# Optimization experiments

Hardware: AMD Instinct MI355X
Metric: run time of the kernel (lower is better)

Reference implementation:

```python
import jax, jax.numpy as jnp
import numpy as np

B_, L_, H_ = 2, 4096, 1024
INTER, NSTATE, NGROUPS, HEADS, P, K, CHUNK = 2048, 128, 1, 32, 64, 4, 256
CONV_DIM = INTER + 2 * NGROUPS * NSTATE  # 2304
PROJ = INTER + CONV_DIM + HEADS          # 4384
LN_EPS = 1e-5


def setup_inputs() -> dict:
    key = jax.random.key(0)
    ks = jax.random.split(key, 8)
    hidden_states = jax.random.normal(ks[0], (B_, L_, H_), jnp.float32)
    in_proj_w = jax.random.normal(ks[1], (PROJ, H_), jnp.float32) * 0.02
    conv_w = jax.random.normal(ks[2], (CONV_DIM, 1, K), jnp.float32) * 0.2
    conv_b = jnp.zeros((CONV_DIM,), jnp.float32)
    # dt_bias init as in module: inv-softplus of dt ~ LogUniform(time_step_min, time_step_max)
    dt = jnp.exp(jax.random.uniform(ks[3], (HEADS,), jnp.float32)
                 * (np.log(0.1) - np.log(0.001)) + np.log(0.001))
    dt = jnp.clip(dt, 1e-4, None)
    dt_bias = dt + jnp.log(-jnp.expm1(-dt))
    A_log = jnp.log(jax.random.uniform(ks[4], (HEADS,), jnp.float32, 1.0, 16.0))
    D = jnp.ones((HEADS,), jnp.float32)
    ln_w = jnp.ones((INTER,), jnp.float32)
    ln_b = jnp.zeros((INTER,), jnp.float32)
    out_proj_w = jax.random.normal(ks[5], (H_, INTER), jnp.float32) * 0.02
    return dict(hidden_states=hidden_states, in_proj_w=in_proj_w, conv_w=conv_w,
                conv_b=conv_b, dt_bias=dt_bias, A_log=A_log, D=D,
                ln_w=ln_w, ln_b=ln_b, out_proj_w=out_proj_w)


def _segsum(x):
    # x [..., c] -> [..., c, c] lower-triangular cumulative segment sums
    T = x.shape[-1]
    cs = jnp.cumsum(x, -1)
    d = cs[..., :, None] - cs[..., None, :]
    mask = jnp.tril(jnp.ones((T, T), bool))
    return jnp.where(mask, d, -jnp.inf)


def _ssd(x, dt, A, Bm, Cm, D):
    # x [b,l,h,p], dt [b,l,h], A [h], Bm/Cm [b,l,h,n] -> y [b,l,h,p]
    b, l, h, p = x.shape
    nc = l // CHUNK
    X = (x * dt[..., None]).reshape(b, nc, CHUNK, h, p)
    Bc = Bm.reshape(b, nc, CHUNK, h, -1)
    Cc = Cm.reshape(b, nc, CHUNK, h, -1)
    dA = (dt * A).reshape(b, nc, CHUNK, h).transpose(0, 3, 1, 2)  # [b,h,nc,c]
    Acs = jnp.cumsum(dA, -1)
    Lm = jnp.exp(_segsum(dA))                                      # [b,h,nc,c,c]
    CB = jnp.einsum("bclhn,bcshn->bhcls", Cc, Bc)
    Yd = jnp.einsum("bhcls,bcshp->bclhp", CB * Lm, X)              # intra-chunk
    decay_states = jnp.exp(Acs[..., -1:] - Acs)                    # [b,h,nc,c]
    states = jnp.einsum("bclhn,bhcl,bclhp->bchpn", Bc, decay_states, X)
    chunk_decay = jnp.exp(Acs[..., -1])                            # [b,h,nc]
    n = Bc.shape[-1]

    def step(carry, inp):
        st, dec = inp
        return carry * dec[..., None, None] + st, carry

    _, prev = jax.lax.scan(step, jnp.zeros((b, h, p, n), x.dtype),
                           (jnp.moveaxis(states, 1, 0), jnp.moveaxis(chunk_decay, 2, 0)))
    prev = jnp.moveaxis(prev, 0, 1)                                # [b,nc,h,p,n]
    Yo = jnp.einsum("bclhn,bchpn,bhcl->bclhp", Cc, prev, jnp.exp(Acs))
    return (Yd + Yo).reshape(b, l, h, p) + D[None, None, :, None] * x


def reference(hidden_states, in_proj_w, conv_w, conv_b, dt_bias, A_log, D,
              ln_w, ln_b, out_proj_w):
    b, l, _ = hidden_states.shape
    proj = hidden_states @ in_proj_w.T                             # [b,l,PROJ]
    gate = proj[..., :INTER]
    xBC = proj[..., INTER:INTER + CONV_DIM]
    dt = jax.nn.softplus(proj[..., INTER + CONV_DIM:] + dt_bias)   # [b,l,heads]
    # depthwise causal conv1d + silu
    xc = jax.lax.conv_general_dilated(xBC.transpose(0, 2, 1), conv_w, (1,),
                                      [(K - 1, 0)], feature_group_count=CONV_DIM,
                                      dimension_numbers=("NCH", "OIH", "NCH"))
    xBC = jax.nn.silu(xc + conv_b[None, :, None]).transpose(0, 2, 1)
    gn = NGROUPS * NSTATE
    x = xBC[..., :INTER].reshape(b, l, HEADS, P)
    Bm = xBC[..., INTER:INTER + gn].reshape(b, l, NGROUPS, NSTATE)
    Cm = xBC[..., INTER + gn:].reshape(b, l, NGROUPS, NSTATE)
    rep = HEADS // NGROUPS
    Bm = jnp.repeat(Bm, rep, axis=2)
    Cm = jnp.repeat(Cm, rep, axis=2)
    A = -jnp.exp(A_log)
    y = _ssd(x, dt, A, Bm, Cm, D).reshape(b, l, INTER)
    mu = y.mean(-1, keepdims=True)
    var = ((y - mu) ** 2).mean(-1, keepdims=True)
    yn = (y - mu) * jax.lax.rsqrt(var + LN_EPS) * ln_w + ln_b
    out = (yn * jax.nn.silu(gate.astype(jnp.float32))) @ out_proj_w.T
    return out
```

## Files before the change

kernel.cpp:

```cpp
#include <hip/hip_runtime.h>

typedef unsigned short u16;
typedef u16 u16x4 __attribute__((ext_vector_type(4)));
typedef u16 u16x8 __attribute__((ext_vector_type(8)));
typedef __bf16 bf16x8 __attribute__((ext_vector_type(8)));
typedef float f32x4 __attribute__((ext_vector_type(4)));

#define B_    2
#define L_    4096
#define H_    1024
#define INTER 2048
#define NSTATE 128
#define HEADS 32
#define P_    64
#define CHUNK 256
#define NC    16
#define CONVD 2304
#define PROJ  4384
#define PROJP 4480
#define XBCW  2432
#define MTOK  8192

__device__ __forceinline__ u16 f2bf(float f) {
  unsigned u = __float_as_uint(f);
  u += 0x7fffu + ((u >> 16) & 1u);
  return (u16)(u >> 16);
}
__device__ __forceinline__ float bf2f(u16 u) {
  return __uint_as_float(((unsigned)u) << 16);
}
__device__ __forceinline__ bf16x8 asbf(u16x8 v) {
  union { u16x8 u; bf16x8 b; } x; x.u = v; return x.b;
}

__global__ void cast_bf16_k(const float* __restrict__ in, u16* __restrict__ out) {
  size_t i = ((size_t)blockIdx.x * 256 + threadIdx.x) * 4;
  float4 v = *(const float4*)(in + i);
  u16x4 o = { f2bf(v.x), f2bf(v.y), f2bf(v.z), f2bf(v.w) };
  *(u16x4*)(out + i) = o;
}

__global__ void cast_w1_k(const float* __restrict__ in, u16* __restrict__ out) {
  size_t i = ((size_t)blockIdx.x * 256 + threadIdx.x) * 4;
  u16x4 o = { 0, 0, 0, 0 };
  if (i < (size_t)PROJ * H_) {
    float4 v = *(const float4*)(in + i);
    o = (u16x4){ f2bf(v.x), f2bf(v.y), f2bf(v.z), f2bf(v.w) };
  }
  *(u16x4*)(out + i) = o;
}

template<int SPLIT>
__global__ __launch_bounds__(256) void gemm_bt_k(
    const u16* __restrict__ A, const u16* __restrict__ Bm, float* __restrict__ C,
    u16* __restrict__ gateb, float* __restrict__ xbcf,
    const int K, const int ldc) {
  __shared__ u16 Als[4096];
  __shared__ u16 Bls[4096];
  const int tid = threadIdx.x;
  const int bn = blockIdx.x, bm = blockIdx.y;
  const u16* Ab = A + (size_t)bm * 128 * K;
  const u16* Bb = Bm + (size_t)bn * 128 * K;
  const int row = tid >> 2, col = (tid & 3) << 3;
  const int lane = tid & 63;
  const int wr = ((tid >> 7) & 1) << 6;
  const int wc = ((tid >> 6) & 1) << 6;
  const int fr = lane & 15;
  const int fk = (lane >> 4) << 3;
  f32x4 acc[4][4] = {};
  const size_t rA0 = (size_t)row * K + col, rA1 = (size_t)(row + 64) * K + col;
  u16x8 ra0 = *(const u16x8*)(Ab + rA0);
  u16x8 ra1 = *(const u16x8*)(Ab + rA1);
  u16x8 rb0 = *(const u16x8*)(Bb + rA0);
  u16x8 rb1 = *(const u16x8*)(Bb + rA1);
  const int nk = K >> 5;
  for (int kt = 0; kt < nk; ++kt) {
    *(u16x8*)(Als + tid * 8) = ra0;
    *(u16x8*)(Als + 2048 + tid * 8) = ra1;
    *(u16x8*)(Bls + tid * 8) = rb0;
    *(u16x8*)(Bls + 2048 + tid * 8) = rb1;
    __syncthreads();
    if (kt + 1 < nk) {
      const size_t ko = (size_t)(kt + 1) * 32;
      ra0 = *(const u16x8*)(Ab + rA0 + ko);
      ra1 = *(const u16x8*)(Ab + rA1 + ko);
      rb0 = *(const u16x8*)(Bb + rA0 + ko);
      rb1 = *(const u16x8*)(Bb + rA1 + ko);
    }
    bf16x8 af[4], bfv[4];
#pragma unroll
    for (int m = 0; m < 4; ++m)
      af[m] = asbf(*(const u16x8*)(Als + (wr + m * 16 + fr) * 32 + fk));
#pragma unroll
    for (int n = 0; n < 4; ++n)
      bfv[n] = asbf(*(const u16x8*)(Bls + (wc + n * 16 + fr) * 32 + fk));
#pragma unroll
    for (int m = 0; m < 4; ++m)
#pragma unroll
      for (int n = 0; n < 4; ++n)
        acc[m][n] = __builtin_amdgcn_mfma_f32_16x16x32_bf16(af[m], bfv[n], acc[m][n], 0, 0, 0);
    __syncthreads();
  }
  const int crow = bm * 128 + wr + ((lane >> 4) << 2);
  if (SPLIT == 0) {
    float* Cp = C + (size_t)crow * ldc + bn * 128 + wc + fr;
#pragma unroll
    for (int m = 0; m < 4; ++m)
#pragma unroll
      for (int n = 0; n < 4; ++n)
#pragma unroll
        for (int j = 0; j < 4; ++j)
          Cp[(size_t)(m * 16 + j) * ldc + n * 16] = acc[m][n][j];
  } else if (bn < 16) {
    u16* Gp = gateb + (size_t)crow * INTER + bn * 128 + wc + fr;
#pragma unroll
    for (int m = 0; m < 4; ++m)
#pragma unroll
      for (int n = 0; n < 4; ++n)
#pragma unroll
        for (int j = 0; j < 4; ++j)
          Gp[(size_t)(m * 16 + j) * INTER + n * 16] = f2bf(acc[m][n][j]);
  } else {
    float* Xp = xbcf + (size_t)crow * XBCW + (bn - 16) * 128 + wc + fr;
#pragma unroll
    for (int m = 0; m < 4; ++m)
#pragma unroll
      for (int n = 0; n < 4; ++n)
#pragma unroll
        for (int j = 0; j < 4; ++j)
          Xp[(size_t)(m * 16 + j) * XBCW + n * 16] = acc[m][n][j];
  }
}

__global__ __launch_bounds__(256) void dtpart_k(
    const float* __restrict__ hs, const float* __restrict__ w1,
    float* __restrict__ part) {
  __shared__ float hls[32 * 256];
  __shared__ float wq[32 * 8 * 32];
  const int ks = blockIdx.x, mt = blockIdx.y;
  const int m0 = mt * 32;
  const int t = threadIdx.x;
  const int h = t & 31, q = t >> 5;
  float w[32];
  {
    const float* wp = w1 + (size_t)(PROJ - HEADS + h) * H_ + ks * 256 + q * 32;
#pragma unroll
    for (int i = 0; i < 8; ++i) {
      const float4 v = *(const float4*)(wp + i * 4);
      w[i * 4] = v.x; w[i * 4 + 1] = v.y; w[i * 4 + 2] = v.z; w[i * 4 + 3] = v.w;
    }
  }
#pragma unroll
  for (int i = 0; i < 8; ++i) {
    const int idx = i * 1024 + t * 4;
    const int row = idx >> 8, col = idx & 255;
    *(float4*)(hls + idx) = *(const float4*)(hs + (size_t)(m0 + row) * H_ + ks * 256 + col);
  }
  __syncthreads();
  for (int tok = 0; tok < 32; ++tok) {
    const float* hp = hls + tok * 256 + q * 32;
    float s = 0.f;
#pragma unroll
    for (int i = 0; i < 8; ++i) {
      const float4 hv = *(const float4*)(hp + i * 4);
      s += w[i * 4] * hv.x + w[i * 4 + 1] * hv.y + w[i * 4 + 2] * hv.z + w[i * 4 + 3] * hv.w;
    }
    wq[tok * 256 + q * 32 + h] = s;
  }
  __syncthreads();
#pragma unroll
  for (int i = 0; i < 4; ++i) {
    const int idx = i * 256 + t;
    const int tok = idx >> 5, h2 = idx & 31;
    float s = 0.f;
#pragma unroll
    for (int qq = 0; qq < 8; ++qq) s += wq[tok * 256 + qq * 32 + h2];
    part[((size_t)ks * MTOK + m0 + tok) * HEADS + h2] = s;
  }
}

__global__ __launch_bounds__(256) void dtfin_k(
    const float* __restrict__ part, const float* __restrict__ dt_bias,
    float* __restrict__ dtb) {
  const int gid = blockIdx.x * 256 + threadIdx.x;
  const int h = gid & 31;
  float z = dt_bias[h];
#pragma unroll
  for (int ks = 0; ks < 4; ++ks) z += part[(size_t)ks * MTOK * HEADS + gid];
  const float sp = z > 0.f ? z + log1pf(__expf(-z)) : log1pf(__expf(z));
  dtb[gid] = sp;
}

__global__ __launch_bounds__(256) void conv_silu_k(
    const float* __restrict__ xbcf, const float* __restrict__ cw,
    const float* __restrict__ cbv,
    u16* __restrict__ xb16, float* __restrict__ Bbuf, float* __restrict__ Cbuf) {
  const int m = blockIdx.x;
  const int l = m & (L_ - 1);
  const int t = threadIdx.x;
  const float* pr = xbcf + (size_t)m * XBCW;
#pragma unroll
  for (int i = 0; i < 9; ++i) {
    const int ch = t + (i << 8);
    float acc = cbv[ch];
    const float* w = cw + ch * 4;
#pragma unroll
    for (int k = 0; k < 4; ++k) {
      const int d = k - 3;
      if (l + d >= 0) acc += w[k] * pr[(long)d * XBCW + ch];
    }
    const float v = acc / (1.f + __expf(-acc));
    if (ch < INTER) xb16[(size_t)m * INTER + ch] = f2bf(v);
    else if (ch < INTER + NSTATE) Bbuf[(size_t)m * NSTATE + (ch - INTER)] = v;
    else Cbuf[(size_t)m * NSTATE + (ch - INTER - NSTATE)] = v;
  }
}

__global__ void dtsum_k(const float* __restrict__ dtb, float* __restrict__ dts) {
  const int idx = blockIdx.x * 256 + threadIdx.x;
  const int h = idx & 31, c = (idx >> 5) & 15, b = idx >> 9;
  const float* p = dtb + (size_t)(b * L_ + c * CHUNK) * HEADS + h;
  float s = 0.f;
  for (int i = 0; i < CHUNK; ++i) s += p[(size_t)i * HEADS];
  dts[idx] = s;
}

__global__ __launch_bounds__(512) void cb_k(
    const float* __restrict__ Bbuf, const float* __restrict__ Cbuf,
    float* __restrict__ CBb) {
  __shared__ u16 Bls[CHUNK * NSTATE];
  const int bx = blockIdx.x;
  const int m0 = bx * CHUNK;
  const int t = threadIdx.x;
#pragma unroll
  for (int i = 0; i < 16; ++i) {
    const int idx = i * 2048 + t * 4;
    const int row = idx >> 7;
    const float4 v = *(const float4*)(Bbuf + (size_t)m0 * NSTATE + idx);
    u16x4 o = { f2bf(v.x), f2bf(v.y), f2bf(v.z), f2bf(v.w) };
    *(u16x4*)(Bls + (idx ^ ((row & 7) << 3))) = o;
  }
  __syncthreads();
  const int lane = t & 63, wv = t >> 6;
  const int fr = lane & 15, fu = lane >> 4;
  u16x8 afrag[2][4];
#pragma unroll
  for (int r = 0; r < 2; ++r) {
    const int row = (wv + r * 8) * 16 + fr;
    const float* cp = Cbuf + (size_t)(m0 + row) * NSTATE + fu * 8;
#pragma unroll
    for (int ks = 0; ks < 4; ++ks) {
      const float4 c0 = *(const float4*)(cp + ks * 32);
      const float4 c1 = *(const float4*)(cp + ks * 32 + 4);
      afrag[r][ks] = (u16x8){ f2bf(c0.x), f2bf(c0.y), f2bf(c0.z), f2bf(c0.w),
                              f2bf(c1.x), f2bf(c1.y), f2bf(c1.z), f2bf(c1.w) };
    }
  }
  for (int ct = 0; ct < 16; ++ct) {
    u16x8 bfrag[4];
#pragma unroll
    for (int ks = 0; ks < 4; ++ks)
      bfrag[ks] = *(const u16x8*)(Bls + (((ct * 16 + fr) * NSTATE + ks * 32 + fu * 8)
                                         ^ ((fr & 7) << 3)));
    f32x4 acc[2] = {};
#pragma unroll
    for (int r = 0; r < 2; ++r)
#pragma unroll
      for (int ks = 0; ks < 4; ++ks)
        acc[r] = __builtin_amdgcn_mfma_f32_16x16x32_bf16(asbf(afrag[r][ks]), asbf(bfrag[ks]), acc[r], 0, 0, 0);
#pragma unroll
    for (int r = 0; r < 2; ++r) {
      const int rowb = (wv + r * 8) * 16 + fu * 4;
#pragma unroll
      for (int reg = 0; reg < 4; ++reg)
        CBb[(size_t)(m0 + rowb + reg) * CHUNK + ct * 16 + fr] = acc[r][reg];
    }
  }
}

__global__ __launch_bounds__(512) void yd_states_k(
    const u16* __restrict__ xb16, const float* __restrict__ Bbuf,
    const float* __restrict__ dtb, const float* __restrict__ CBb,
    const float* __restrict__ A_log, u16* __restrict__ ydb16,
    float* __restrict__ states) {
  __shared__ float acs[CHUNK];
  __shared__ float dec[CHUNK];
  __shared__ u16 Xt[P_ * CHUNK];
  const int bx = blockIdx.x;
  const int h = bx & 31, c = (bx >> 5) & 15, b = bx >> 9;
  const int t = threadIdx.x;
  const int m0 = b * L_ + c * CHUNK;
  const float Ah = -__expf(A_log[h]);
  if (t < CHUNK) acs[t] = dtb[(size_t)(m0 + t) * HEADS + h];
  __syncthreads();
  {
#pragma unroll
    for (int i = 0; i < 4; ++i) {
      const int s = i * 64 + (t >> 3);
      const int p0 = (t & 7) * 8;
      const float dtv = acs[s];
      const u16x8 v = *(const u16x8*)(xb16 + (size_t)(m0 + s) * INTER + h * P_ + p0);
#pragma unroll
      for (int j = 0; j < 8; ++j)
        Xt[((p0 + j) * CHUNK + s) ^ (j << 3)] = f2bf(bf2f(v[j]) * dtv);
    }
  }
  for (int off = 1; off < CHUNK; off <<= 1) {
    float add = 0.f;
    if (t >= off && t < CHUNK) add = acs[t - off];
    __syncthreads();
    if (t >= off && t < CHUNK) acs[t] += add;
    __syncthreads();
  }
  {
    const float cum = (t < CHUNK) ? acs[t] : 0.f;
    const float tot = acs[CHUNK - 1];
    __syncthreads();
    if (t < CHUNK) {
      acs[t] = Ah * cum;
      dec[t] = __expf(Ah * (tot - cum));
    }
    __syncthreads();
  }
  const int lane = t & 63;
  const int wv = t >> 6;
  const int fr = lane & 15;
  const int fu = lane >> 4;
  {
    f32x4 acc_st[4] = {};
    const float* Bg = Bbuf + (size_t)m0 * NSTATE + wv * 16 + fr;
#pragma unroll 2
    for (int ks = 0; ks < 8; ++ks) {
      const int s0 = ks * 32 + fu * 8;
      u16x8 bw;
#pragma unroll
      for (int j = 0; j < 8; ++j)
        bw[j] = f2bf(Bg[(size_t)(s0 + j) * NSTATE] * dec[s0 + j]);
#pragma unroll
      for (int pt = 0; pt < 4; ++pt) {
        const int p = pt * 16 + fr;
        const u16x8 xa = *(const u16x8*)(Xt + ((p * CHUNK + s0) ^ ((p & 7) << 3)));
        acc_st[pt] = __builtin_amdgcn_mfma_f32_16x16x32_bf16(asbf(xa), asbf(bw), acc_st[pt], 0, 0, 0);
      }
    }
    float* sp = states + (size_t)((b * NC + c) * HEADS + h) * (P_ * NSTATE);
#pragma unroll
    for (int pt = 0; pt < 4; ++pt)
#pragma unroll
      for (int reg = 0; reg < 4; ++reg)
        sp[(size_t)(pt * 16 + fu * 4 + reg) * NSTATE + wv * 16 + fr] = acc_st[pt][reg];
  }
  {
#pragma unroll
    for (int rep = 0; rep < 2; ++rep) {
      const int lt = rep ? (15 - wv) : wv;
      const int l = lt * 16 + fr;
      const float acl = acs[l];
      const float* cbr = CBb + (size_t)(m0 + l) * CHUNK;
      f32x4 acc_yd[4] = {};
      const int ksn = (lt >> 1) + 1;
      for (int ks = 0; ks < ksn; ++ks) {
        const int s0 = ks * 32 + fu * 8;
        const float4 cb0 = *(const float4*)(cbr + s0);
        const float4 cb1 = *(const float4*)(cbr + s0 + 4);
        u16x8 w8;
#pragma unroll
        for (int j = 0; j < 8; ++j) {
          const int s = s0 + j;
          const float cb = j < 4 ? ((const float*)&cb0)[j] : ((const float*)&cb1)[j - 4];
          const float w = (s <= l) ? cb * __expf(acl - acs[s]) : 0.f;
          w8[j] = f2bf(w);
        }
#pragma unroll
        for (int pt = 0; pt < 4; ++pt) {
          const int p = pt * 16 + fr;
          const u16x8 xb = *(const u16x8*)(Xt + ((p * CHUNK + s0) ^ ((p & 7) << 3)));
          acc_yd[pt] = __builtin_amdgcn_mfma_f32_16x16x32_bf16(asbf(w8), asbf(xb), acc_yd[pt], 0, 0, 0);
        }
      }
#pragma unroll
      for (int pt = 0; pt < 4; ++pt)
#pragma unroll
        for (int reg = 0; reg < 4; ++reg)
          ydb16[(size_t)(m0 + lt * 16 + fu * 4 + reg) * INTER + h * P_ + pt * 16 + fr] =
              f2bf(acc_yd[pt][reg]);
    }
  }
}

__global__ void scan_k(const float* __restrict__ states, const float* __restrict__ dts,
                       const float* __restrict__ A_log, u16* __restrict__ prevb) {
  const int gid = blockIdx.x * 256 + threadIdx.x;
  const int b = gid >> 18;
  const int h = (gid >> 13) & 31;
  const int pn = gid & 8191;
  const float Ah = -__expf(A_log[h]);
  float carry = 0.f;
  const size_t base = (size_t)b * (NC * HEADS * P_ * NSTATE) + (size_t)h * (P_ * NSTATE) + pn;
  const float* sp = states + base;
  u16* pp = prevb + base;
  for (int c = 0; c < NC; ++c) {
    const float dcv = __expf(Ah * dts[(b * NC + c) * HEADS + h]);
    const float st = sp[(size_t)c * (HEADS * P_ * NSTATE)];
    pp[(size_t)c * (HEADS * P_ * NSTATE)] = f2bf(carry);
    carry = carry * dcv + st;
  }
}

__global__ __launch_bounds__(512) void yo_final_k(
    const u16* __restrict__ xb16, const float* __restrict__ Cbuf,
    const float* __restrict__ dtb, const u16* __restrict__ prevb,
    const float* __restrict__ A_log, const float* __restrict__ Dv,
    const u16* __restrict__ ydb16, u16* __restrict__ ybf) {
  __shared__ float acs[CHUNK];
  const int bx = blockIdx.x;
  const int h = bx & 31, c = (bx >> 5) & 15, b = bx >> 9;
  const int t = threadIdx.x;
  const int m0 = b * L_ + c * CHUNK;
  const float Ah = -__expf(A_log[h]);
  const float Dh = Dv[h];
  if (t < CHUNK) acs[t] = dtb[(size_t)(m0 + t) * HEADS + h];
  __syncthreads();
  for (int off = 1; off < CHUNK; off <<= 1) {
    float add = 0.f;
    if (t >= off && t < CHUNK) add = acs[t - off];
    __syncthreads();
    if (t >= off && t < CHUNK) acs[t] += add;
    __syncthreads();
  }
  const int lane = t & 63;
  const int wv = t >> 6;
  const int fr = lane & 15;
  const int fu = lane >> 4;
  const u16* pb = prevb + (size_t)((b * NC + c) * HEADS + h) * (P_ * NSTATE);
  u16x8 bfrag[4][4];
#pragma unroll
  for (int pt = 0; pt < 4; ++pt)
#pragma unroll
    for (int ks = 0; ks < 4; ++ks)
      bfrag[pt][ks] = *(const u16x8*)(pb + (pt * 16 + fr) * NSTATE + ks * 32 + fu * 8);
#pragma unroll
  for (int rep = 0; rep < 2; ++rep) {
    const int lt = rep * 8 + wv;
    const float* cr = Cbuf + (size_t)(m0 + lt * 16 + fr) * NSTATE + fu * 8;
    f32x4 acc[4] = {};
#pragma unroll
    for (int ks = 0; ks < 4; ++ks) {
      const float4 c0 = *(const float4*)(cr + ks * 32);
      const float4 c1 = *(const float4*)(cr + ks * 32 + 4);
      const u16x8 a8 = { f2bf(c0.x), f2bf(c0.y), f2bf(c0.z), f2bf(c0.w),
                         f2bf(c1.x), f2bf(c1.y), f2bf(c1.z), f2bf(c1.w) };
#pragma unroll
      for (int pt = 0; pt < 4; ++pt)
        acc[pt] = __builtin_amdgcn_mfma_f32_16x16x32_bf16(asbf(a8), asbf(bfrag[pt][ks]), acc[pt], 0, 0, 0);
    }
#pragma unroll
    for (int reg = 0; reg < 4; ++reg) {
      const int l = lt * 16 + fu * 4 + reg;
      const float el = __expf(Ah * acs[l]);
      const size_t base = (size_t)(m0 + l) * INTER + h * P_;
#pragma unroll
      for (int pt = 0; pt < 4; ++pt) {
        const int p = pt * 16 + fr;
        const float yd = bf2f(ydb16[base + p]);
        const float xv = bf2f(xb16[base + p]);
        ybf[base + p] = f2bf(yd + el * acc[pt][reg] + Dh * xv);
      }
    }
  }
}

__global__ __launch_bounds__(256) void ln_gate_k(
    const u16* __restrict__ ybf, const u16* __restrict__ gateb,
    const float* __restrict__ lnw, const float* __restrict__ lnb,
    u16* __restrict__ yact) {
  __shared__ float red[8];
  const int m = blockIdx.x, t = threadIdx.x;
  const u16x8 yv = *(const u16x8*)(ybf + (size_t)m * INTER + t * 8);
  float y[8];
  float s = 0.f, ss = 0.f;
#pragma unroll
  for (int j = 0; j < 8; ++j) { y[j] = bf2f(yv[j]); s += y[j]; ss += y[j] * y[j]; }
#pragma unroll
  for (int off = 32; off > 0; off >>= 1) {
    s += __shfl_xor(s, off);
    ss += __shfl_xor(ss, off);
  }
  if ((t & 63) == 0) { red[(t >> 6) * 2] = s; red[(t >> 6) * 2 + 1] = ss; }
  __syncthreads();
  s = red[0] + red[2] + red[4] + red[6];
  ss = red[1] + red[3] + red[5] + red[7];
  const float mu = s * (1.f / INTER);
  const float rs = rsqrtf(ss * (1.f / INTER) - mu * mu + 1e-5f);
  const u16x8 gv = *(const u16x8*)(gateb + (size_t)m * INTER + t * 8);
  const float4 w0 = *(const float4*)(lnw + t * 8);
  const float4 w1 = *(const float4*)(lnw + t * 8 + 4);
  const float4 b0 = *(const float4*)(lnb + t * 8);
  const float4 b1 = *(const float4*)(lnb + t * 8 + 4);
  const float wj[8] = { w0.x, w0.y, w0.z, w0.w, w1.x, w1.y, w1.z, w1.w };
  const float bj[8] = { b0.x, b0.y, b0.z, b0.w, b1.x, b1.y, b1.z, b1.w };
  u16x8 o;
#pragma unroll
  for (int j = 0; j < 8; ++j) {
    const float g = bf2f(gv[j]);
    const float yn = (y[j] - mu) * rs * wj[j] + bj[j];
    const float sg = g / (1.f + __expf(-g));
    o[j] = f2bf(yn * sg);
  }
  *(u16x8*)(yact + (size_t)m * INTER + t * 8) = o;
}

extern "C" void kernel_launch(void* const* d_in, const int* in_sizes, int n_in,
                              void* d_out, int out_size, void* d_ws, size_t ws_size,
                              hipStream_t stream) {
  (void)in_sizes; (void)n_in; (void)out_size; (void)ws_size;
  const float* hs     = (const float*)d_in[0];
  const float* w1     = (const float*)d_in[1];
  const float* cw     = (const float*)d_in[2];
  const float* cbv    = (const float*)d_in[3];
  const float* dtbias = (const float*)d_in[4];
  const float* alog   = (const float*)d_in[5];
  const float* Dv     = (const float*)d_in[6];
  const float* lnw    = (const float*)d_in[7];
  const float* lnb    = (const float*)d_in[8];
  const float* w2     = (const float*)d_in[9];
  float* out = (float*)d_out;
  char* ws = (char*)d_ws;
  size_t off = 0;
  auto alloc = [&](size_t bytes) {
    void* p = ws + off; off += (bytes + 255) & ~(size_t)255; return p;
  };
  u16*   hb     = (u16*)alloc((size_t)MTOK * H_ * 2);
  float* CBb    = (float*)hb;
  u16*   prevb  = hb;
  u16*   w1b    = (u16*)alloc((size_t)PROJP * H_ * 2);
  u16*   w2b    = (u16*)alloc((size_t)H_ * INTER * 2);
  u16*   gateb  = (u16*)alloc((size_t)MTOK * INTER * 2);
  float* xbcf   = (float*)alloc((size_t)MTOK * XBCW * 4);
  u16*   ydb16  = (u16*)xbcf;
  u16*   ybf    = (u16*)((char*)xbcf + ((size_t)MTOK * INTER * 2));
  u16*   xb16   = (u16*)alloc((size_t)MTOK * INTER * 2);
  u16*   yact   = xb16;
  float* Bbuf   = (float*)alloc((size_t)MTOK * NSTATE * 4);
  float* Cbuf   = (float*)alloc((size_t)MTOK * NSTATE * 4);
  float* dtb    = (float*)alloc((size_t)MTOK * HEADS * 4);
  float* dts    = (float*)alloc(1024 * 4);
  float* states = (float*)alloc((size_t)B_ * NC * HEADS * P_ * NSTATE * 4);
  float* part   = states;

  cast_bf16_k<<<MTOK * H_ / 1024, 256, 0, stream>>>(hs, hb);
  cast_w1_k<<<PROJP * H_ / 1024, 256, 0, stream>>>(w1, w1b);
  cast_bf16_k<<<H_ * INTER / 1024, 256, 0, stream>>>(w2, w2b);
  dtpart_k<<<dim3(4, MTOK / 32), 256, 0, stream>>>(hs, w1, part);
  dtfin_k<<<MTOK * HEADS / 256, 256, 0, stream>>>(part, dtbias, dtb);
  gemm_bt_k<1><<<dim3(PROJP / 128, MTOK / 128), 256, 0, stream>>>(
      hb, w1b, nullptr, gateb, xbcf, H_, 0);
  conv_silu_k<<<MTOK, 256, 0, stream>>>(xbcf, cw, cbv, xb16, Bbuf, Cbuf);
  dtsum_k<<<4, 256, 0, stream>>>(dtb, dts);
  cb_k<<<B_ * NC, 512, 0, stream>>>(Bbuf, Cbuf, CBb);
  yd_states_k<<<B_ * NC * HEADS, 512, 0, stream>>>(xb16, Bbuf, dtb, CBb, alog, ydb16, states);
  scan_k<<<B_ * HEADS * P_ * NSTATE / 256, 256, 0, stream>>>(states, dts, alog, prevb);
  yo_final_k<<<B_ * NC * HEADS, 512, 0, stream>>>(xb16, Cbuf, dtb, prevb, alog, Dv, ydb16, ybf);
  ln_gate_k<<<MTOK, 256, 0, stream>>>(ybf, gateb, lnw, lnb, yact);
  gemm_bt_k<0><<<dim3(H_ / 128, MTOK / 128), 256, 0, stream>>>(
      yact, w2b, out, nullptr, nullptr, INTER, H_);
}
```

Measured before the change: 501.4 us.

## Pad GEMM LDS rows, swizzle block order, store xBC intermediate as bf16

After: 501.9 us. No clear change (+0.1%).

```diff
diff --git a/kernel.cpp b/kernel.cpp
--- a/kernel.cpp
+++ b/kernel.cpp
@@ -20,6 +20,7 @@
 #define PROJP 4480
 #define XBCW  2432
 #define MTOK  8192
+#define LDSW  40
 
 __device__ __forceinline__ u16 f2bf(float f) {
   unsigned u = __float_as_uint(f);
@@ -53,12 +54,16 @@
 template<int SPLIT>
 __global__ __launch_bounds__(256) void gemm_bt_k(
     const u16* __restrict__ A, const u16* __restrict__ Bm, float* __restrict__ C,
-    u16* __restrict__ gateb, float* __restrict__ xbcf,
+    u16* __restrict__ gateb, u16* __restrict__ xbcb,
     const int K, const int ldc) {
-  __shared__ u16 Als[4096];
-  __shared__ u16 Bls[4096];
+  __shared__ u16 Als[128 * LDSW];
+  __shared__ u16 Bls[128 * LDSW];
   const int tid = threadIdx.x;
-  const int bn = blockIdx.x, bm = blockIdx.y;
+  const int nbx = gridDim.x;
+  const int nwg = nbx * gridDim.y;
+  const int bid = blockIdx.y * nbx + blockIdx.x;
+  const int swz = (bid & 7) * (nwg >> 3) + (bid >> 3);
+  const int bn = swz % nbx, bm = swz / nbx;
   const u16* Ab = A + (size_t)bm * 128 * K;
   const u16* Bb = Bm + (size_t)bn * 128 * K;
   const int row = tid >> 2, col = (tid & 3) << 3;
@@ -74,11 +79,12 @@
   u16x8 rb0 = *(const u16x8*)(Bb + rA0);
   u16x8 rb1 = *(const u16x8*)(Bb + rA1);
   const int nk = K >> 5;
+  const int wofs = row * LDSW + col;
   for (int kt = 0; kt < nk; ++kt) {
-    *(u16x8*)(Als + tid * 8) = ra0;
-    *(u16x8*)(Als + 2048 + tid * 8) = ra1;
-    *(u16x8*)(Bls + tid * 8) = rb0;
-    *(u16x8*)(Bls + 2048 + tid * 8) = rb1;
+    *(u16x8*)(Als + wofs) = ra0;
+    *(u16x8*)(Als + 64 * LDSW + wofs) = ra1;
+    *(u16x8*)(Bls + wofs) = rb0;
+    *(u16x8*)(Bls + 64 * LDSW + wofs) = rb1;
     __syncthreads();
     if (kt + 1 < nk) {
       const size_t ko = (size_t)(kt + 1) * 32;
@@ -90,10 +96,10 @@
     bf16x8 af[4], bfv[4];
 #pragma unroll
     for (int m = 0; m < 4; ++m)
-      af[m] = asbf(*(const u16x8*)(Als + (wr + m * 16 + fr) * 32 + fk));
+      af[m] = asbf(*(const u16x8*)(Als + (wr + m * 16 + fr) * LDSW + fk));
 #pragma unroll
     for (int n = 0; n < 4; ++n)
-      bfv[n] = asbf(*(const u16x8*)(Bls + (wc + n * 16 + fr) * 32 + fk));
+      bfv[n] = asbf(*(const u16x8*)(Bls + (wc + n * 16 + fr) * LDSW + fk));
 #pragma unroll
     for (int m = 0; m < 4; ++m)
 #pragma unroll
@@ -121,14 +127,14 @@
         for (int j = 0; j < 4; ++j)
           Gp[(size_t)(m * 16 + j) * INTER + n * 16] = f2bf(acc[m][n][j]);
   } else {
-    float* Xp = xbcf + (size_t)crow * XBCW + (bn - 16) * 128 + wc + fr;
+    u16* Xp = xbcb + (size_t)crow * XBCW + (bn - 16) * 128 + wc + fr;
 #pragma unroll
     for (int m = 0; m < 4; ++m)
 #pragma unroll
       for (int n = 0; n < 4; ++n)
 #pragma unroll
         for (int j = 0; j < 4; ++j)
-          Xp[(size_t)(m * 16 + j) * XBCW + n * 16] = acc[m][n][j];
+          Xp[(size_t)(m * 16 + j) * XBCW + n * 16] = f2bf(acc[m][n][j]);
   }
 }
 
@@ -192,13 +198,13 @@
 }
 
 __global__ __launch_bounds__(256) void conv_silu_k(
-    const float* __restrict__ xbcf, const float* __restrict__ cw,
+    const u16* __restrict__ xbcb, const float* __restrict__ cw,
     const float* __restrict__ cbv,
     u16* __restrict__ xb16, float* __restrict__ Bbuf, float* __restrict__ Cbuf) {
   const int m = blockIdx.x;
   const int l = m & (L_ - 1);
   const int t = threadIdx.x;
-  const float* pr = xbcf + (size_t)m * XBCW;
+  const u16* pr = xbcb + (size_t)m * XBCW;
 #pragma unroll
   for (int i = 0; i < 9; ++i) {
     const int ch = t + (i << 8);
@@ -207,7 +213,7 @@
 #pragma unroll
     for (int k = 0; k < 4; ++k) {
       const int d = k - 3;
-      if (l + d >= 0) acc += w[k] * pr[(long)d * XBCW + ch];
+      if (l + d >= 0) acc += w[k] * bf2f(pr[(long)d * XBCW + ch]);
     }
     const float v = acc / (1.f + __expf(-acc));
     if (ch < INTER) xb16[(size_t)m * INTER + ch] = f2bf(v);
@@ -536,9 +542,9 @@
   u16*   w1b    = (u16*)alloc((size_t)PROJP * H_ * 2);
   u16*   w2b    = (u16*)alloc((size_t)H_ * INTER * 2);
   u16*   gateb  = (u16*)alloc((size_t)MTOK * INTER * 2);
-  float* xbcf   = (float*)alloc((size_t)MTOK * XBCW * 4);
-  u16*   ydb16  = (u16*)xbcf;
-  u16*   ybf    = (u16*)((char*)xbcf + ((size_t)MTOK * INTER * 2));
+  u16*   xbcb   = (u16*)alloc((size_t)MTOK * XBCW * 2);
+  u16*   ydb16  = xbcb;
+  u16*   ybf    = (u16*)alloc((size_t)MTOK * INTER * 2);
   u16*   xb16   = (u16*)alloc((size_t)MTOK * INTER * 2);
   u16*   yact   = xb16;
   float* Bbuf   = (float*)alloc((size_t)MTOK * NSTATE * 4);
@@ -554,8 +560,8 @@
   dtpart_k<<<dim3(4, MTOK / 32), 256, 0, stream>>>(hs, w1, part);
   dtfin_k<<<MTOK * HEADS / 256, 256, 0, stream>>>(part, dtbias, dtb);
   gemm_bt_k<1><<<dim3(PROJP / 128, MTOK / 128), 256, 0, stream>>>(
-      hb, w1b, nullptr, gateb, xbcf, H_, 0);
-  conv_silu_k<<<MTOK, 256, 0, stream>>>(xbcf, cw, cbv, xb16, Bbuf, Cbuf);
+      hb, w1b, nullptr, gateb, xbcb, H_, 0);
+  conv_silu_k<<<MTOK, 256, 0, stream>>>(xbcb, cw, cbv, xb16, Bbuf, Cbuf);
   dtsum_k<<<4, 256, 0, stream>>>(dtb, dts);
   cb_k<<<B_ * NC, 512, 0, stream>>>(Bbuf, Cbuf, CBb);
   yd_states_k<<<B_ * NC * HEADS, 512, 0, stream>>>(xb16, Bbuf, dtb, CBb, alog, ydb16, states);
```
